# Performance work log

Measured on AMD Instinct MI355X. Metric: run time of the kernel, lower is better.

Reference implementation:

```python
import jax, jax.numpy as jnp
import numpy as np

NUM_HEADS = 8
OUT_FEATS = 128
D_HEAD = OUT_FEATS // NUM_HEADS
N_NODES = 50000
N_EDGES = 600000
IN_FEATS = 128


def setup_inputs() -> dict:
    key = jax.random.key(0)
    ks = jax.random.split(key, 10)
    h = jax.random.normal(ks[0], (N_NODES, IN_FEATS), dtype=jnp.float32)
    src = jax.random.randint(ks[1], (N_EDGES,), 0, N_NODES)
    dst = jax.random.randint(ks[2], (N_EDGES,), 0, N_NODES)
    s = 1.0 / np.sqrt(IN_FEATS)
    W_Q = jax.random.normal(ks[3], (IN_FEATS, OUT_FEATS), dtype=jnp.float32) * s
    W_K = jax.random.normal(ks[4], (IN_FEATS, OUT_FEATS), dtype=jnp.float32) * s
    W_V = jax.random.normal(ks[5], (IN_FEATS, OUT_FEATS), dtype=jnp.float32) * s
    b_Q = jnp.zeros((OUT_FEATS,), dtype=jnp.float32)
    b_K = jnp.zeros((OUT_FEATS,), dtype=jnp.float32)
    b_V = jnp.zeros((OUT_FEATS,), dtype=jnp.float32)
    return {"h": h, "W_Q": W_Q, "b_Q": b_Q, "W_K": W_K, "b_K": b_K,
            "W_V": W_V, "b_V": b_V, "src": src, "dst": dst}


def _graph_conv(h, W, b, src, dst, norm_src, norm_dst):
    # DGL GraphConv, norm='both': D_dst^{-1/2} * A * D_src^{-1/2} * (h W) + b
    x = (h * norm_src[:, None]) @ W                              # [N, F]
    agg = jax.ops.segment_sum(x[src], dst, num_segments=h.shape[0])
    return agg * norm_dst[:, None] + b


def reference(h, W_Q, b_Q, W_K, b_K, W_V, b_V, src, dst):
    N = h.shape[0]
    ones = jnp.ones(src.shape[0], dtype=h.dtype)
    deg_out = jax.ops.segment_sum(ones, src, num_segments=N)   # out-degree (src side)
    deg_in = jax.ops.segment_sum(ones, dst, num_segments=N)    # in-degree (dst side)
    norm_src = jax.lax.rsqrt(jnp.clip(deg_out, 1.0))
    norm_dst = jax.lax.rsqrt(jnp.clip(deg_in, 1.0))

    Q = jax.nn.relu(_graph_conv(h, W_Q, b_Q, src, dst, norm_src, norm_dst))
    K = jax.nn.relu(_graph_conv(h, W_K, b_K, src, dst, norm_src, norm_dst))
    V = jax.nn.relu(_graph_conv(h, W_V, b_V, src, dst, norm_src, norm_dst))

    Qh = Q.reshape(N, NUM_HEADS, D_HEAD)
    Kh = K.reshape(N, NUM_HEADS, D_HEAD)
    Vh = V.reshape(N, NUM_HEADS, D_HEAD)

    # edge-wise scores: K at src dotted with Q at dst, per head
    score = jnp.sum(Kh[src] * Qh[dst], axis=-1, keepdims=True)   # [E, H, 1]
    score = jnp.exp(jnp.clip(score / np.sqrt(D_HEAD), -10.0, 10.0))

    wV = jax.ops.segment_sum(Vh[src] * score, dst, num_segments=N)  # [N, H, Dh]
    z = jax.ops.segment_sum(score, dst, num_segments=N)             # [N, H, 1]
    return wV / (z + 1e-6)
```

## Files before the change

kernel.cpp:

```cpp
#include <hip/hip_runtime.h>

#define INF  128
#define OUTF 128
#define NH   8
#define DHD  16
#define CAP  48

typedef __attribute__((ext_vector_type(8))) short bf16x8;
typedef __attribute__((ext_vector_type(4))) float f32x4;

__device__ __forceinline__ float bf16_to_f32(unsigned short u) {
    union { unsigned int i; float f; } v;
    v.i = ((unsigned int)u) << 16;
    return v.f;
}
__device__ __forceinline__ unsigned short f32_to_bf16(float f) {
    union { float f; unsigned int i; } v;
    v.f = f;
    unsigned int x = v.i;
    return (unsigned short)((x + 0x7fffu + ((x >> 16) & 1u)) >> 16);
}

__global__ void k_front(const int* __restrict__ src, const int* __restrict__ dst,
                        int* __restrict__ deg_out, int* __restrict__ cursor,
                        int* __restrict__ edge_src, int E, int SB, int HB,
                        const float* __restrict__ h, unsigned short* __restrict__ h_b, int N,
                        const float* __restrict__ Wq, const float* __restrict__ Wk,
                        const float* __restrict__ Wv, unsigned short* __restrict__ frag) {
    if (blockIdx.x < (unsigned)SB) {
        int t = blockIdx.x * 256 + threadIdx.x;
        int e0 = t * 4;
        if (e0 + 4 <= E) {
            int4 s4 = *reinterpret_cast<const int4*>(src + e0);
            int4 d4 = *reinterpret_cast<const int4*>(dst + e0);
            atomicAdd(&deg_out[s4.x], 1);
            atomicAdd(&deg_out[s4.y], 1);
            atomicAdd(&deg_out[s4.z], 1);
            atomicAdd(&deg_out[s4.w], 1);
            int p0 = atomicAdd(&cursor[d4.x], 1);
            int p1 = atomicAdd(&cursor[d4.y], 1);
            int p2 = atomicAdd(&cursor[d4.z], 1);
            int p3 = atomicAdd(&cursor[d4.w], 1);
            if (p0 < CAP) edge_src[d4.x * CAP + p0] = s4.x;
            if (p1 < CAP) edge_src[d4.y * CAP + p1] = s4.y;
            if (p2 < CAP) edge_src[d4.z * CAP + p2] = s4.z;
            if (p3 < CAP) edge_src[d4.w * CAP + p3] = s4.w;
        } else {
            for (int e = e0; e < E; ++e) {
                int s = src[e];
                int d = dst[e];
                atomicAdd(&deg_out[s], 1);
                int p = atomicAdd(&cursor[d], 1);
                if (p < CAP) edge_src[d * CAP + p] = s;
            }
        }
    } else if (blockIdx.x < (unsigned)(SB + HB)) {
        int t = (blockIdx.x - SB) * 256 + threadIdx.x;
        if (t < N * (INF / 8)) {
            const float4* p = reinterpret_cast<const float4*>(h + (size_t)t * 8);
            float4 v0 = p[0], v1 = p[1];
            uint4 o;
            o.x = (unsigned int)f32_to_bf16(v0.x) | ((unsigned int)f32_to_bf16(v0.y) << 16);
            o.y = (unsigned int)f32_to_bf16(v0.z) | ((unsigned int)f32_to_bf16(v0.w) << 16);
            o.z = (unsigned int)f32_to_bf16(v1.x) | ((unsigned int)f32_to_bf16(v1.y) << 16);
            o.w = (unsigned int)f32_to_bf16(v1.z) | ((unsigned int)f32_to_bf16(v1.w) << 16);
            *reinterpret_cast<uint4*>(h_b + (size_t)t * 8) = o;
        }
    } else {
        int t = (blockIdx.x - SB - HB) * 256 + threadIdx.x;
        if (t >= 3 * 8 * 4 * 2 * 64) return;
        int lane  = t & 63;
        int plane = (t >> 6) & 1;
        int ks    = (t >> 7) & 3;
        int nt    = (t >> 9) & 7;
        int mat   = t >> 12;
        const float* W = (mat == 0) ? Wq : ((mat == 1) ? Wk : Wv);
        int ln = lane & 15, quad = lane >> 4;
        int n = nt * 16 + ln;
        unsigned short vals[8];
        #pragma unroll
        for (int j = 0; j < 8; ++j) {
            int k = ks * 32 + quad * 8 + j;
            float a = W[k * OUTF + n];
            unsigned short hb = f32_to_bf16(a);
            vals[j] = plane ? f32_to_bf16(a - bf16_to_f32(hb)) : hb;
        }
        unsigned int* dp = reinterpret_cast<unsigned int*>(frag + (size_t)t * 8);
        #pragma unroll
        for (int j = 0; j < 4; ++j)
            dp[j] = (unsigned int)vals[2 * j] | ((unsigned int)vals[2 * j + 1] << 16);
    }
}

__global__ __launch_bounds__(256) void k_agg(const unsigned short* __restrict__ h_b,
                                             const int* __restrict__ deg_out,
                                             const int* __restrict__ cursor,
                                             const int* __restrict__ edge_src,
                                             float* __restrict__ agg, int N) {
    int wid  = (blockIdx.x * 256 + threadIdx.x) >> 6;
    int lane = threadIdx.x & 63;
    if (wid >= N) return;
    int half = lane >> 5, li = lane & 31;
    int c4 = li * 4;
    float a0 = 0.f, a1 = 0.f, a2 = 0.f, a3 = 0.f;
    int deg = cursor[wid]; if (deg > CAP) deg = CAP;
    const int* row = edge_src + wid * CAP;
    auto proc = [&](int e) {
        int s = row[e];
        int dg = deg_out[s]; if (dg < 1) dg = 1;
        float ns = rsqrtf((float)dg);
        uint2 p = *reinterpret_cast<const uint2*>(h_b + (size_t)s * INF + c4);
        a0 += ns * bf16_to_f32((unsigned short)(p.x & 0xffffu));
        a1 += ns * bf16_to_f32((unsigned short)(p.x >> 16));
        a2 += ns * bf16_to_f32((unsigned short)(p.y & 0xffffu));
        a3 += ns * bf16_to_f32((unsigned short)(p.y >> 16));
    };
    int e = half;
    for (; e + 4 <= deg; e += 4) { proc(e); proc(e + 2); }
    for (; e < deg; e += 2) proc(e);
    a0 += __shfl_xor(a0, 32);
    a1 += __shfl_xor(a1, 32);
    a2 += __shfl_xor(a2, 32);
    a3 += __shfl_xor(a3, 32);
    if (half == 0)
        *reinterpret_cast<float4*>(agg + (size_t)wid * INF + c4) =
            make_float4(a0, a1, a2, a3);
}

__global__ __launch_bounds__(256) void k_gemm(const float* __restrict__ agg,
                                              const unsigned short* __restrict__ frag,
                                              const float* __restrict__ bq,
                                              const float* __restrict__ bk,
                                              const float* __restrict__ bv,
                                              const int* __restrict__ cursor,
                                              float* __restrict__ qbuf,
                                              unsigned short* __restrict__ kvbuf,
                                              int N) {
    int mat = blockIdx.y;
    const float* bb = (mat == 0) ? bq : ((mat == 1) ? bk : bv);

    int wave = threadIdx.x >> 6;
    int lane = threadIdx.x & 63;
    int ln   = lane & 15;
    int quad = lane >> 4;
    int mrow = blockIdx.x * 64 + wave * 16;

    bf16x8 ah[4], al[4];
    {
        int m = mrow + ln; if (m >= N) m = N - 1;
        const float* arow = agg + (size_t)m * INF;
        #pragma unroll
        for (int ks = 0; ks < 4; ++ks) {
            const float4* p = reinterpret_cast<const float4*>(arow + ks * 32 + quad * 8);
            float4 v0 = p[0], v1 = p[1];
            float vv[8] = {v0.x, v0.y, v0.z, v0.w, v1.x, v1.y, v1.z, v1.w};
            #pragma unroll
            for (int j = 0; j < 8; ++j) {
                unsigned short hb = f32_to_bf16(vv[j]);
                ah[ks][j] = (short)hb;
                al[ks][j] = (short)f32_to_bf16(vv[j] - bf16_to_f32(hb));
            }
        }
    }

    float nrm[4];
    #pragma unroll
    for (int r = 0; r < 4; ++r) {
        int m = mrow + quad * 4 + r;
        if (m < N) {
            int dg = cursor[m]; if (dg < 1) dg = 1;
            nrm[r] = rsqrtf((float)dg);
        } else nrm[r] = 0.f;
    }

    #pragma unroll 2
    for (int nt = 0; nt < 8; ++nt) {
        int n0 = nt * 16;
        f32x4 acc = {0.f, 0.f, 0.f, 0.f};
        #pragma unroll
        for (int ks = 0; ks < 4; ++ks) {
            size_t base = ((size_t)(((mat * 8 + nt) * 4 + ks) * 2) * 64 + lane) * 8;
            bf16x8 bh = *reinterpret_cast<const bf16x8*>(frag + base);
            bf16x8 bl = *reinterpret_cast<const bf16x8*>(frag + base + 64 * 8);
            acc = __builtin_amdgcn_mfma_f32_16x16x32_bf16(ah[ks], bh, acc, 0, 0, 0);
            acc = __builtin_amdgcn_mfma_f32_16x16x32_bf16(al[ks], bh, acc, 0, 0, 0);
            acc = __builtin_amdgcn_mfma_f32_16x16x32_bf16(ah[ks], bl, acc, 0, 0, 0);
        }
        int col = n0 + ln;
        float bias = bb[col];
        #pragma unroll
        for (int r = 0; r < 4; ++r) {
            int m = mrow + quad * 4 + r;
            if (m < N) {
                float v = acc[r] * nrm[r] + bias;
                v = (v > 0.f) ? v : 0.f;
                if (mat == 0) {
                    qbuf[(size_t)m * OUTF + col] = v;
                } else {
                    int idx = ((col >> 2) << 3) + (col & 3) + ((mat == 2) ? 4 : 0);
                    kvbuf[(size_t)m * 2 * OUTF + idx] = f32_to_bf16(v);
                }
            }
        }
    }
}

__global__ __launch_bounds__(256) void k_attn(const float* __restrict__ qbuf,
                                              const unsigned short* __restrict__ kvbuf,
                                              const int* __restrict__ cursor,
                                              const int* __restrict__ edge_src,
                                              float* __restrict__ out, int N) {
    int wid  = (blockIdx.x * 256 + threadIdx.x) >> 6;
    int lane = threadIdx.x & 63;
    if (wid >= N) return;
    int half = lane >> 5, li = lane & 31;
    int c4 = li * 4;
    float4 q = *reinterpret_cast<const float4*>(qbuf + (size_t)wid * OUTF + c4);
    float a0 = 0.f, a1 = 0.f, a2 = 0.f, a3 = 0.f, z = 0.f;
    int deg = cursor[wid]; if (deg > CAP) deg = CAP;
    const int* row = edge_src + wid * CAP;
    auto proc = [&](int e) {
        int s = row[e];
        uint4 kp = *reinterpret_cast<const uint4*>(kvbuf + (size_t)s * 2 * OUTF + li * 8);
        float p = q.x * bf16_to_f32((unsigned short)(kp.x & 0xffffu))
                + q.y * bf16_to_f32((unsigned short)(kp.x >> 16))
                + q.z * bf16_to_f32((unsigned short)(kp.y & 0xffffu))
                + q.w * bf16_to_f32((unsigned short)(kp.y >> 16));
        p += __shfl_xor(p, 1);
        p += __shfl_xor(p, 2);
        float w = __expf(fminf(fmaxf(0.25f * p, -10.f), 10.f));
        z  += w;
        a0 += w * bf16_to_f32((unsigned short)(kp.z & 0xffffu));
        a1 += w * bf16_to_f32((unsigned short)(kp.z >> 16));
        a2 += w * bf16_to_f32((unsigned short)(kp.w & 0xffffu));
        a3 += w * bf16_to_f32((unsigned short)(kp.w >> 16));
    };
    int e = half;
    for (; e + 4 <= deg; e += 4) { proc(e); proc(e + 2); }
    for (; e < deg; e += 2) proc(e);
    a0 += __shfl_xor(a0, 32);
    a1 += __shfl_xor(a1, 32);
    a2 += __shfl_xor(a2, 32);
    a3 += __shfl_xor(a3, 32);
    z  += __shfl_xor(z, 32);
    if (half == 0) {
        float inv = 1.0f / (z + 1e-6f);
        *reinterpret_cast<float4*>(out + (size_t)wid * OUTF + c4) =
            make_float4(a0 * inv, a1 * inv, a2 * inv, a3 * inv);
    }
}

extern "C" void kernel_launch(void* const* d_in, const int* in_sizes, int n_in,
                              void* d_out, int out_size, void* d_ws, size_t ws_size,
                              hipStream_t stream) {
    const float* h  = (const float*)d_in[0];
    const float* Wq = (const float*)d_in[1];
    const float* bq = (const float*)d_in[2];
    const float* Wk = (const float*)d_in[3];
    const float* bk = (const float*)d_in[4];
    const float* Wv = (const float*)d_in[5];
    const float* bv = (const float*)d_in[6];
    const int* src = (const int*)d_in[7];
    const int* dst = (const int*)d_in[8];

    const int N = in_sizes[0] / INF;
    const int E = in_sizes[7];

    char* ws = (char*)d_ws;
    size_t off = 0;
    auto carve = [&](size_t bytes) -> void* {
        void* p = ws + off;
        off = (off + bytes + 255) & ~(size_t)255;
        return p;
    };
    int*   zeroed    = (int*)  carve((size_t)2 * N * sizeof(int));
    int*   deg_out   = zeroed;
    int*   cursor    = zeroed + N;
    int*   edge_src  = (int*)  carve((size_t)N * CAP * sizeof(int));
    unsigned short* h_b  = (unsigned short*)carve((size_t)N * INF * sizeof(unsigned short));
    float* agg       = (float*)carve((size_t)N * INF * sizeof(float));
    float* qbuf      = (float*)carve((size_t)N * OUTF * sizeof(float));
    unsigned short* kvbuf = (unsigned short*)carve((size_t)N * 2 * OUTF * sizeof(unsigned short));
    unsigned short* wfrag = (unsigned short*)carve((size_t)3 * 8 * 4 * 2 * 64 * 8 * sizeof(unsigned short));
    (void)ws_size;

    float* out = (float*)d_out;

    hipMemsetAsync(zeroed, 0, (size_t)2 * N * sizeof(int), stream);

    int SB = (E / 4 + 255) / 256 + 1;
    int HB = (N * (INF / 8) + 255) / 256;
    int WB = (3 * 8 * 4 * 2 * 64 + 255) / 256;
    k_front<<<SB + HB + WB, 256, 0, stream>>>(src, dst, deg_out, cursor, edge_src,
                                              E, SB, HB, h, h_b, N, Wq, Wk, Wv, wfrag);

    int gAgg = (N + 3) / 4;
    k_agg<<<gAgg, 256, 0, stream>>>(h_b, deg_out, cursor, edge_src, agg, N);

    dim3 gemm_grid((N + 63) / 64, 3);
    k_gemm<<<gemm_grid, 256, 0, stream>>>(agg, wfrag, bq, bk, bv,
                                          cursor, qbuf, kvbuf, N);

    k_attn<<<gAgg, 256, 0, stream>>>(qbuf, kvbuf, cursor, edge_src, out, N);
}
```

Before: 277.8 us.

## Privatize degree histograms and edge buckets per XCD with workgroup-scope atomics

Splits the degree counters and CSR-style edge buckets into eight per-XCD copies, chosen by the hardware XCC ID register, so atomics can use workgroup scope and stay in the local L2 instead of going device-wide. A new merge kernel sums the partial degrees into precomputed norm_src/norm_dst arrays, which the aggregation and GEMM kernels now read instead of recomputing rsqrt from degrees. The agg and attention kernels walk the eight sub-buckets through per-lane offset tables, which costs a larger memset, more index arithmetic per edge and an extra launch. Workgroup-scope atomics on global memory across blocks on the same XCD rely on hardware behaviour, and the per-partition cap of 16 may silently drop edges for busy destinations.

```diff
diff --git a/kernel.cpp b/kernel.cpp
--- a/kernel.cpp
+++ b/kernel.cpp
@@ -4,7 +4,8 @@
 #define OUTF 128
 #define NH   8
 #define DHD  16
-#define CAP  48
+#define NXCD 8
+#define CAPP 16
 
 typedef __attribute__((ext_vector_type(8))) short bf16x8;
 typedef __attribute__((ext_vector_type(4))) float f32x4;
@@ -21,37 +22,47 @@
     return (unsigned short)((x + 0x7fffu + ((x >> 16) & 1u)) >> 16);
 }
 
+__device__ __forceinline__ int atom_inc_xcd(int* p) {
+    return __hip_atomic_fetch_add(p, 1, __ATOMIC_RELAXED, __HIP_MEMORY_SCOPE_WORKGROUP);
+}
+
 __global__ void k_front(const int* __restrict__ src, const int* __restrict__ dst,
-                        int* __restrict__ deg_out, int* __restrict__ cursor,
-                        int* __restrict__ edge_src, int E, int SB, int HB,
-                        const float* __restrict__ h, unsigned short* __restrict__ h_b, int N,
+                        int* __restrict__ deg_out_p, int* __restrict__ cursor_p,
+                        int* __restrict__ edge_src_p, int E, int N, int SB, int HB,
+                        const float* __restrict__ h, unsigned short* __restrict__ h_b,
                         const float* __restrict__ Wq, const float* __restrict__ Wk,
                         const float* __restrict__ Wv, unsigned short* __restrict__ frag) {
     if (blockIdx.x < (unsigned)SB) {
+        unsigned xr;
+        asm("s_getreg_b32 %0, hwreg(HW_REG_XCC_ID)" : "=s"(xr));
+        int xcd = (int)(xr & 7u);
+        int* degp = deg_out_p + (size_t)xcd * N;
+        int* curp = cursor_p  + (size_t)xcd * N;
+        int* esp  = edge_src_p + (size_t)xcd * N * CAPP;
         int t = blockIdx.x * 256 + threadIdx.x;
         int e0 = t * 4;
         if (e0 + 4 <= E) {
             int4 s4 = *reinterpret_cast<const int4*>(src + e0);
             int4 d4 = *reinterpret_cast<const int4*>(dst + e0);
-            atomicAdd(&deg_out[s4.x], 1);
-            atomicAdd(&deg_out[s4.y], 1);
-            atomicAdd(&deg_out[s4.z], 1);
-            atomicAdd(&deg_out[s4.w], 1);
-            int p0 = atomicAdd(&cursor[d4.x], 1);
-            int p1 = atomicAdd(&cursor[d4.y], 1);
-            int p2 = atomicAdd(&cursor[d4.z], 1);
-            int p3 = atomicAdd(&cursor[d4.w], 1);
-            if (p0 < CAP) edge_src[d4.x * CAP + p0] = s4.x;
-            if (p1 < CAP) edge_src[d4.y * CAP + p1] = s4.y;
-            if (p2 < CAP) edge_src[d4.z * CAP + p2] = s4.z;
-            if (p3 < CAP) edge_src[d4.w * CAP + p3] = s4.w;
+            atom_inc_xcd(&degp[s4.x]);
+            atom_inc_xcd(&degp[s4.y]);
+            atom_inc_xcd(&degp[s4.z]);
+            atom_inc_xcd(&degp[s4.w]);
+            int p0 = atom_inc_xcd(&curp[d4.x]);
+            int p1 = atom_inc_xcd(&curp[d4.y]);
+            int p2 = atom_inc_xcd(&curp[d4.z]);
+            int p3 = atom_inc_xcd(&curp[d4.w]);
+            if (p0 < CAPP) esp[d4.x * CAPP + p0] = s4.x;
+            if (p1 < CAPP) esp[d4.y * CAPP + p1] = s4.y;
+            if (p2 < CAPP) esp[d4.z * CAPP + p2] = s4.z;
+            if (p3 < CAPP) esp[d4.w * CAPP + p3] = s4.w;
         } else {
             for (int e = e0; e < E; ++e) {
                 int s = src[e];
                 int d = dst[e];
-                atomicAdd(&deg_out[s], 1);
-                int p = atomicAdd(&cursor[d], 1);
-                if (p < CAP) edge_src[d * CAP + p] = s;
+                atom_inc_xcd(&degp[s]);
+                int p = atom_inc_xcd(&curp[d]);
+                if (p < CAPP) esp[d * CAPP + p] = s;
             }
         }
     } else if (blockIdx.x < (unsigned)(SB + HB)) {
@@ -92,32 +103,60 @@
     }
 }
 
+__global__ __launch_bounds__(256) void k_merge(const int* __restrict__ deg_out_p,
+                                               const int* __restrict__ cursor_p,
+                                               float* __restrict__ norm_src,
+                                               float* __restrict__ norm_dst, int N) {
+    int v = blockIdx.x * 256 + threadIdx.x;
+    if (v >= N) return;
+    int so = 0, si = 0;
+    #pragma unroll
+    for (int p = 0; p < NXCD; ++p) {
+        so += deg_out_p[(size_t)p * N + v];
+        si += cursor_p[(size_t)p * N + v];
+    }
+    if (so < 1) so = 1;
+    if (si < 1) si = 1;
+    norm_src[v] = rsqrtf((float)so);
+    norm_dst[v] = rsqrtf((float)si);
+}
+
 __global__ __launch_bounds__(256) void k_agg(const unsigned short* __restrict__ h_b,
-                                             const int* __restrict__ deg_out,
-                                             const int* __restrict__ cursor,
-                                             const int* __restrict__ edge_src,
+                                             const float* __restrict__ norm_src,
+                                             const int* __restrict__ cursor_p,
+                                             const int* __restrict__ edge_src_p,
                                              float* __restrict__ agg, int N) {
     int wid  = (blockIdx.x * 256 + threadIdx.x) >> 6;
     int lane = threadIdx.x & 63;
     if (wid >= N) return;
     int half = lane >> 5, li = lane & 31;
     int c4 = li * 4;
+    int cnt[NXCD], off[NXCD], tot = 0;
+    #pragma unroll
+    for (int p = 0; p < NXCD; ++p) {
+        int c = cursor_p[(size_t)p * N + wid];
+        if (c > CAPP) c = CAPP;
+        off[p] = tot; tot += c; cnt[p] = c;
+    }
     float a0 = 0.f, a1 = 0.f, a2 = 0.f, a3 = 0.f;
-    int deg = cursor[wid]; if (deg > CAP) deg = CAP;
-    const int* row = edge_src + wid * CAP;
     auto proc = [&](int e) {
-        int s = row[e];
-        int dg = deg_out[s]; if (dg < 1) dg = 1;
-        float ns = rsqrtf((float)dg);
-        uint2 p = *reinterpret_cast<const uint2*>(h_b + (size_t)s * INF + c4);
-        a0 += ns * bf16_to_f32((unsigned short)(p.x & 0xffffu));
-        a1 += ns * bf16_to_f32((unsigned short)(p.x >> 16));
-        a2 += ns * bf16_to_f32((unsigned short)(p.y & 0xffffu));
-        a3 += ns * bf16_to_f32((unsigned short)(p.y >> 16));
+        int psel = 0, l = e;
+        #pragma unroll
+        for (int p = 0; p < NXCD; ++p) {
+            bool in = (e >= off[p]) && (e - off[p] < cnt[p]);
+            if (in) { psel = p; l = e - off[p]; }
+        }
+        int s = edge_src_p[((size_t)psel * N + wid) * CAPP + l];
+        float ns = norm_src[s];
+        uint2 pch = *reinterpret_cast<const uint2*>(h_b + (size_t)s * INF + c4);
+        a0 += ns * bf16_to_f32((unsigned short)(pch.x & 0xffffu));
+        a1 += ns * bf16_to_f32((unsigned short)(pch.x >> 16));
+        a2 += ns * bf16_to_f32((unsigned short)(pch.y & 0xffffu));
+        a3 += ns * bf16_to_f32((unsigned short)(pch.y >> 16));
     };
     int e = half;
-    for (; e + 4 <= deg; e += 4) { proc(e); proc(e + 2); }
-    for (; e < deg; e += 2) proc(e);
+    for (; e + 4 <= tot; e += 4) { proc(e); proc(e + 2); }
+    for (; e < tot; e += 2) proc(e);
     a0 += __shfl_xor(a0, 32);
     a1 += __shfl_xor(a1, 32);
     a2 += __shfl_xor(a2, 32);
@@ -132,7 +171,7 @@
                                               const float* __restrict__ bq,
                                               const float* __restrict__ bk,
                                               const float* __restrict__ bv,
-                                              const int* __restrict__ cursor,
+                                              const float* __restrict__ norm_dst,
                                               float* __restrict__ qbuf,
                                               unsigned short* __restrict__ kvbuf,
                                               int N) {
@@ -167,10 +206,7 @@
     #pragma unroll
     for (int r = 0; r < 4; ++r) {
         int m = mrow + quad * 4 + r;
-        if (m < N) {
-            int dg = cursor[m]; if (dg < 1) dg = 1;
-            nrm[r] = rsqrtf((float)dg);
-        } else nrm[r] = 0.f;
+        nrm[r] = (m < N) ? norm_dst[m] : 0.f;
     }
 
     #pragma unroll 2
@@ -207,8 +243,8 @@
 
 __global__ __launch_bounds__(256) void k_attn(const float* __restrict__ qbuf,
                                               const unsigned short* __restrict__ kvbuf,
-                                              const int* __restrict__ cursor,
-                                              const int* __restrict__ edge_src,
+                                              const int* __restrict__ cursor_p,
+                                              const int* __restrict__ edge_src_p,
                                               float* __restrict__ out, int N) {
     int wid  = (blockIdx.x * 256 + threadIdx.x) >> 6;
     int lane = threadIdx.x & 63;
@@ -216,19 +252,30 @@
     int half = lane >> 5, li = lane & 31;
     int c4 = li * 4;
     float4 q = *reinterpret_cast<const float4*>(qbuf + (size_t)wid * OUTF + c4);
+    int cnt[NXCD], off[NXCD], tot = 0;
+    #pragma unroll
+    for (int p = 0; p < NXCD; ++p) {
+        int c = cursor_p[(size_t)p * N + wid];
+        if (c > CAPP) c = CAPP;
+        off[p] = tot; tot += c; cnt[p] = c;
+    }
     float a0 = 0.f, a1 = 0.f, a2 = 0.f, a3 = 0.f, z = 0.f;
-    int deg = cursor[wid]; if (deg > CAP) deg = CAP;
-    const int* row = edge_src + wid * CAP;
     auto proc = [&](int e) {
-        int s = row[e];
+        int psel = 0, l = e;
+        #pragma unroll
+        for (int p = 0; p < NXCD; ++p) {
+            bool in = (e >= off[p]) && (e - off[p] < cnt[p]);
+            if (in) { psel = p; l = e - off[p]; }
+        }
+        int s = edge_src_p[((size_t)psel * N + wid) * CAPP + l];
         uint4 kp = *reinterpret_cast<const uint4*>(kvbuf + (size_t)s * 2 * OUTF + li * 8);
-        float p = q.x * bf16_to_f32((unsigned short)(kp.x & 0xffffu))
-                + q.y * bf16_to_f32((unsigned short)(kp.x >> 16))
-                + q.z * bf16_to_f32((unsigned short)(kp.y & 0xffffu))
-                + q.w * bf16_to_f32((unsigned short)(kp.y >> 16));
-        p += __shfl_xor(p, 1);
-        p += __shfl_xor(p, 2);
-        float w = __expf(fminf(fmaxf(0.25f * p, -10.f), 10.f));
+        float p_ = q.x * bf16_to_f32((unsigned short)(kp.x & 0xffffu))
+                 + q.y * bf16_to_f32((unsigned short)(kp.x >> 16))
+                 + q.z * bf16_to_f32((unsigned short)(kp.y & 0xffffu))
+                 + q.w * bf16_to_f32((unsigned short)(kp.y >> 16));
+        p_ += __shfl_xor(p_, 1);
+        p_ += __shfl_xor(p_, 2);
+        float w = __expf(fminf(fmaxf(0.25f * p_, -10.f), 10.f));
         z  += w;
         a0 += w * bf16_to_f32((unsigned short)(kp.z & 0xffffu));
         a1 += w * bf16_to_f32((unsigned short)(kp.z >> 16));
@@ -236,8 +283,8 @@
         a3 += w * bf16_to_f32((unsigned short)(kp.w >> 16));
     };
     int e = half;
-    for (; e + 4 <= deg; e += 4) { proc(e); proc(e + 2); }
-    for (; e < deg; e += 2) proc(e);
+    for (; e + 4 <= tot; e += 4) { proc(e); proc(e + 2); }
+    for (; e < tot; e += 2) proc(e);
     a0 += __shfl_xor(a0, 32);
     a1 += __shfl_xor(a1, 32);
     a2 += __shfl_xor(a2, 32);
@@ -273,33 +320,37 @@
         off = (off + bytes + 255) & ~(size_t)255;
         return p;
     };
-    int*   zeroed    = (int*)  carve((size_t)2 * N * sizeof(int));
-    int*   deg_out   = zeroed;
-    int*   cursor    = zeroed + N;
-    int*   edge_src  = (int*)  carve((size_t)N * CAP * sizeof(int));
+    int* hist       = (int*)carve((size_t)2 * NXCD * N * sizeof(int));
+    int* deg_out_p  = hist;
+    int* cursor_p   = hist + (size_t)NXCD * N;
+    int* edge_src_p = (int*)carve((size_t)NXCD * N * CAPP * sizeof(int));
+    float* norm_src = (float*)carve((size_t)N * sizeof(float));
+    float* norm_dst = (float*)carve((size_t)N * sizeof(float));
     unsigned short* h_b  = (unsigned short*)carve((size_t)N * INF * sizeof(unsigned short));
-    float* agg       = (float*)carve((size_t)N * INF * sizeof(float));
-    float* qbuf      = (float*)carve((size_t)N * OUTF * sizeof(float));
+    float* agg      = (float*)carve((size_t)N * INF * sizeof(float));
+    float* qbuf     = (float*)carve((size_t)N * OUTF * sizeof(float));
     unsigned short* kvbuf = (unsigned short*)carve((size_t)N * 2 * OUTF * sizeof(unsigned short));
     unsigned short* wfrag = (unsigned short*)carve((size_t)3 * 8 * 4 * 2 * 64 * 8 * sizeof(unsigned short));
     (void)ws_size;
 
     float* out = (float*)d_out;
 
-    hipMemsetAsync(zeroed, 0, (size_t)2 * N * sizeof(int), stream);
+    hipMemsetAsync(hist, 0, (size_t)2 * NXCD * N * sizeof(int), stream);
 
     int SB = (E / 4 + 255) / 256 + 1;
     int HB = (N * (INF / 8) + 255) / 256;
     int WB = (3 * 8 * 4 * 2 * 64 + 255) / 256;
-    k_front<<<SB + HB + WB, 256, 0, stream>>>(src, dst, deg_out, cursor, edge_src,
-                                              E, SB, HB, h, h_b, N, Wq, Wk, Wv, wfrag);
+    k_front<<<SB + HB + WB, 256, 0, stream>>>(src, dst, deg_out_p, cursor_p, edge_src_p,
+                                              E, N, SB, HB, h, h_b, Wq, Wk, Wv, wfrag);
+
+    k_merge<<<(N + 255) / 256, 256, 0, stream>>>(deg_out_p, cursor_p, norm_src, norm_dst, N);
 
     int gAgg = (N + 3) / 4;
-    k_agg<<<gAgg, 256, 0, stream>>>(h_b, deg_out, cursor, edge_src, agg, N);
+    k_agg<<<gAgg, 256, 0, stream>>>(h_b, norm_src, cursor_p, edge_src_p, agg, N);
 
     dim3 gemm_grid((N + 63) / 64, 3);
     k_gemm<<<gemm_grid, 256, 0, stream>>>(agg, wfrag, bq, bk, bv,
-                                          cursor, qbuf, kvbuf, N);
-
-    k_attn<<<gAgg, 256, 0, stream>>>(qbuf, kvbuf, cursor, edge_src, out, N);
-}
+                                          norm_dst, qbuf, kvbuf, N);
+
+    k_attn<<<gAgg, 256, 0, stream>>>(qbuf, kvbuf, cursor_p, edge_src_p, out, N);
+}
```

New measurement: 302.6 us. 1.09x slower.
